# Kernel tuning notes

Hardware: AMD Instinct MI355X
Metric: run time of the kernel (lower is better)

Reference implementation:

```python
import jax, jax.numpy as jnp
import numpy as np

K, D_IN, D_OUT, R = 64, 256, 256, 64
TOK_PER_E = 4096
N_TOK = K * TOK_PER_E


def setup_inputs() -> dict:
    key = jax.random.key(0)
    k1, k2, k3, k4 = jax.random.split(key, 4)
    inp = jax.random.normal(k1, (N_TOK, D_IN), jnp.float32)
    # kaiming-uniform-ish scale for expert weights
    weight = jax.random.normal(k2, (K, D_OUT, D_IN), jnp.float32) * (1.0 / np.sqrt(D_IN))
    bias = jax.random.normal(k3, (K, D_OUT), jnp.float32) * 0.02
    # c_psuedo_inv built exactly as in __init__ from components [k, d, r]
    components = jax.random.normal(k4, (K, D_OUT, R), jnp.float32)
    gram = jnp.einsum('kdr,kds->krs', components, components)          # [k, r, r]
    c_inv = jnp.linalg.inv(gram)
    c_psuedo_inv = jnp.einsum('kdr,krs,kds->kds', components, c_inv, components)  # [k, d, d]
    fwd_expert_count = jnp.full((K,), TOK_PER_E, dtype=jnp.int32)
    return {
        'inp': inp,
        'fwd_expert_count': fwd_expert_count,
        'weight': weight,
        'bias': bias,
        'c_psuedo_inv': c_psuedo_inv,
        'max_tokens': TOK_PER_E,
    }


def reference(inp, fwd_expert_count, weight, bias, c_psuedo_inv, max_tokens):
    counts = fwd_expert_count                      # [k]
    k = counts.shape[0]
    n = inp.shape[0]
    offsets = jnp.concatenate([jnp.zeros((1,), counts.dtype), jnp.cumsum(counts)])  # [k+1]
    expert_ids = jnp.repeat(jnp.arange(k, dtype=counts.dtype), counts,
                            total_repeat_length=n)                                   # [n]
    token_pos = jnp.arange(n, dtype=counts.dtype) - offsets[expert_ids]              # [n]

    # Scatter ragged tokens into padded [k, max_tokens, in_feat], then do the
    # grouped linear as one batched GEMM (padded rows are zero; masked after bias).
    padded_in = jnp.zeros((k, max_tokens, inp.shape[1]), inp.dtype)
    padded_in = padded_in.at[expert_ids, token_pos].set(inp)
    x_pad = jnp.einsum('ktd,ked->kte', padded_in, weight) + bias[:, None, :]         # [k, t, e]
    valid = (jnp.arange(max_tokens)[None, :] < counts[:, None])[..., None]
    x_pad = jnp.where(valid, x_pad, jnp.zeros((), x_pad.dtype))

    padded = jnp.transpose(x_pad, (1, 0, 2))                                         # [t, k, e]
    return jnp.einsum('nkd,kds->nks', padded, c_psuedo_inv)                          # [t, k, e]
```

## Files before the change

kernel.cpp:

```cpp
#include <hip/hip_runtime.h>
#include <hip/hip_bf16.h>
#include <stdint.h>


typedef unsigned int   u32;
typedef unsigned short u16;

typedef short bf16x8 __attribute__((ext_vector_type(8)));
typedef float f32x4  __attribute__((ext_vector_type(4)));

__device__ __forceinline__ bf16x8 pack8(const float* v) {
  union { __hip_bfloat16 h[8]; bf16x8 v8; } r;
#pragma unroll
  for (int j = 0; j < 8; ++j) r.h[j] = __float2bfloat16(v[j]);
  return r.v8;
}
__device__ __forceinline__ u16 f2bf1(float f) {
  union { __hip_bfloat16 h; u16 u; } r;
  r.h = __float2bfloat16(f);
  return r.u;
}
__device__ __forceinline__ u32 pk2(float a, float b) {
  union { __hip_bfloat162 h; u32 u; } r;
  r.h.x = __float2bfloat16(a);
  r.h.y = __float2bfloat16(b);
  return r.u;
}
__device__ __forceinline__ void gload_lds16(const void* g, void* l) {
  __builtin_amdgcn_global_load_lds((__attribute__((address_space(1))) void*)g,
                                   (__attribute__((address_space(3))) void*)l,
                                   16, 0, 0);
}

__global__ __launch_bounds__(256, 2) void k_m(const float* __restrict__ P,
                                              const float* __restrict__ W,
                                              const float* __restrict__ bias,
                                              u16* __restrict__ Mt,
                                              float* __restrict__ b2) {
  const int k = blockIdx.y;
  const int tid = threadIdx.x;
  __shared__ __align__(16) unsigned char LDS[65536];
  const float* Pk = P + (size_t)k * 16384;

  if (blockIdx.x == 4) {
    const int sq = tid & 15, ec = tid >> 4;
    const float* bk = bias + k * 256;
    f32x4 acc = {};
#pragma unroll
    for (int i = 0; i < 16; ++i) {
      const int e = ec * 16 + i;
      const float4 pv = *reinterpret_cast<const float4*>(Pk + (size_t)e * 64 + sq * 4);
      const float bv = bk[e];
      acc[0] = fmaf(bv, pv.x, acc[0]);
      acc[1] = fmaf(bv, pv.y, acc[1]);
      acc[2] = fmaf(bv, pv.z, acc[2]);
      acc[3] = fmaf(bv, pv.w, acc[3]);
    }
    float* red = reinterpret_cast<float*>(LDS);
    *reinterpret_cast<f32x4*>(red + ec * 64 + sq * 4) = acc;
    __syncthreads();
    if (tid < 64) {
      float sum = 0.f;
#pragma unroll
      for (int c = 0; c < 16; ++c) sum += red[c * 64 + tid];
      b2[k * 64 + tid] = sum;
    }
    return;
  }

  const int d0 = blockIdx.x * 64;
  u32* WT = reinterpret_cast<u32*>(LDS);
  u32* PT = reinterpret_cast<u32*>(LDS + 32768);
  const float* Wk = W + (size_t)k * 65536;
  const int lane = tid & 63, w = tid >> 6, q = lane & 15, g = lane >> 4;

#pragma unroll
  for (int r = 0; r < 8; ++r) {
    const int ep = r * 16 + w * 4 + g;
    const float4 w0 = *reinterpret_cast<const float4*>(Wk + (size_t)(2 * ep) * 256 + d0 + 4 * q);
    const float4 w1 = *reinterpret_cast<const float4*>(Wk + (size_t)(2 * ep + 1) * 256 + d0 + 4 * q);
    const float4 p0 = *reinterpret_cast<const float4*>(Pk + (size_t)(2 * ep) * 64 + 4 * q);
    const float4 p1 = *reinterpret_cast<const float4*>(Pk + (size_t)(2 * ep + 1) * 64 + 4 * q);
    const int c = ep >> 2, cw = ep & 3;
    const float wa[4] = {w0.x, w0.y, w0.z, w0.w};
    const float wb[4] = {w1.x, w1.y, w1.z, w1.w};
    const float pa[4] = {p0.x, p0.y, p0.z, p0.w};
    const float pb[4] = {p1.x, p1.y, p1.z, p1.w};
#pragma unroll
    for (int j = 0; j < 4; ++j) {
      const int rw = 4 * q + j;
      const int sc = c ^ (rw & 7);
      WT[rw * 128 + sc * 4 + cw] = pk2(wa[j], wb[j]);
      PT[rw * 128 + sc * 4 + cw] = pk2(pa[j], pb[j]);
    }
  }
  __syncthreads();

  f32x4 acc[4] = {};
  const int dl = w * 16 + q;
#pragma unroll
  for (int kk = 0; kk < 8; ++kk) {
    const bf16x8 bfr = *reinterpret_cast<const bf16x8*>(
        reinterpret_cast<const char*>(WT) + dl * 512 + (((kk * 4 + g) ^ (dl & 7)) * 16));
#pragma unroll
    for (int m = 0; m < 4; ++m) {
      const int s = m * 16 + q;
      const bf16x8 afr = *reinterpret_cast<const bf16x8*>(
          reinterpret_cast<const char*>(PT) + s * 512 + (((kk * 4 + g) ^ (s & 7)) * 16));
      acc[m] = __builtin_amdgcn_mfma_f32_16x16x32_bf16(afr, bfr, acc[m], 0, 0, 0);
    }
  }
  u16* Mk = Mt + (size_t)k * 16384;
#pragma unroll
  for (int m = 0; m < 4; ++m)
#pragma unroll
    for (int j = 0; j < 4; ++j) {
      const int s = m * 16 + g * 4 + j;
      Mk[(size_t)s * 256 + d0 + w * 16 + q] = f2bf1(acc[m][j]);
    }
}

__global__ __launch_bounds__(256, 4) void k_main(const float* __restrict__ inp,
                                                 const u16* __restrict__ Mt,
                                                 const float* __restrict__ b2,
                                                 float* __restrict__ out) {
  const int tb = blockIdx.x, k = blockIdx.y;
  const int tid = threadIdx.x, lane = tid & 63, w = tid >> 6;
  __shared__ __align__(16) u16 Bl[16384];
  const u16* Mk = Mt + (size_t)k * 16384;
#pragma unroll
  for (int r = 0; r < 8; ++r) {
    const int q = r * 256 + tid;
    const int s = q >> 5, u = q & 31;
    gload_lds16(Mk + (size_t)s * 256 + ((u ^ (s & 7)) * 8),
                (char*)Bl + r * 4096 + w * 1024);
  }
  const float* Ak = inp + ((size_t)k * 4096 + tb * 256 + w * 64) * 256;
  f32x4 acc[4][4] = {};
  __syncthreads();

#pragma unroll
  for (int kk = 0; kk < 8; ++kk) {
    bf16x8 mt[4];
#pragma unroll
    for (int n = 0; n < 4; ++n) {
      const int s = n * 16 + (lane & 15);
      const int u = kk * 4 + (lane >> 4);
      mt[n] = *reinterpret_cast<const bf16x8*>(
          (const char*)Bl + s * 512 + ((u ^ (s & 7)) * 16));
    }
#pragma unroll
    for (int m = 0; m < 4; ++m) {
      const float* ap = Ak + (size_t)(m * 16 + (lane & 15)) * 256 +
                        kk * 32 + (lane >> 4) * 8;
      float va[8];
      *reinterpret_cast<float4*>(&va[0]) = *reinterpret_cast<const float4*>(ap);
      *reinterpret_cast<float4*>(&va[4]) = *reinterpret_cast<const float4*>(ap + 4);
      bf16x8 a = pack8(va);
#pragma unroll
      for (int n = 0; n < 4; ++n)
        acc[m][n] = __builtin_amdgcn_mfma_f32_16x16x32_bf16(mt[n], a, acc[m][n], 0, 0, 0);
    }
  }

  const float* b2k = b2 + k * 64;
  const int T0 = tb * 256 + w * 64;
  float4 bv[4];
#pragma unroll
  for (int n = 0; n < 4; ++n)
    bv[n] = *reinterpret_cast<const float4*>(b2k + n * 16 + (lane >> 4) * 4);
#pragma unroll
  for (int m = 0; m < 4; ++m) {
    const int t = T0 + m * 16 + (lane & 15);
    float* op = out + (size_t)t * 4096 + k * 64;
#pragma unroll
    for (int n = 0; n < 4; ++n) {
      float4 r;
      r.x = acc[m][n][0] + bv[n].x;
      r.y = acc[m][n][1] + bv[n].y;
      r.z = acc[m][n][2] + bv[n].z;
      r.w = acc[m][n][3] + bv[n].w;
      *reinterpret_cast<float4*>(op + n * 16 + (lane >> 4) * 4) = r;
    }
  }
}

extern "C" void kernel_launch(void* const* d_in, const int* in_sizes, int n_in,
                              void* d_out, int out_size, void* d_ws, size_t ws_size,
                              hipStream_t stream) {
  const float* inp  = (const float*)d_in[0];
  const float* W    = (const float*)d_in[2];
  const float* bias = (const float*)d_in[3];
  const float* P    = (const float*)d_in[4];

  u16*   Mm = (u16*)d_ws;
  float* b2 = (float*)((char*)d_ws + 2097152);
  float* o  = (float*)d_out;

  k_m   <<<dim3(5, 64),  256, 0, stream>>>(P, W, bias, Mm, b2);
  k_main<<<dim3(16, 64), 256, 0, stream>>>(inp, Mm, b2, o);
}
```

Measured before the change: 89.96 us.

## Stage input tiles through double-buffered LDS via async loads in main kernel

The main kernel now loads the fp32 input tile into LDS with global_load_lds, in 64-column chunks double-buffered across four stages, so the next chunk's fetch overlaps MFMA on the current one. Before, each lane issued direct global loads on the critical path. Each block now handles 64 tokens instead of 256, giving a 4x larger grid, a smaller accumulator, and 64KB of LDS per block with occupancy lowered to 2. The cost is a barrier per stage and the M matrix being reloaded into LDS four times as often overall.

```diff
diff --git a/kernel.cpp b/kernel.cpp
--- a/kernel.cpp
+++ b/kernel.cpp
@@ -120,68 +120,79 @@
     }
 }
 
-__global__ __launch_bounds__(256, 4) void k_main(const float* __restrict__ inp,
+__global__ __launch_bounds__(256, 2) void k_main(const float* __restrict__ inp,
                                                  const u16* __restrict__ Mt,
                                                  const float* __restrict__ b2,
                                                  float* __restrict__ out) {
   const int tb = blockIdx.x, k = blockIdx.y;
   const int tid = threadIdx.x, lane = tid & 63, w = tid >> 6;
-  __shared__ __align__(16) u16 Bl[16384];
+  const int q = lane & 15, g = lane >> 4;
+  __shared__ __align__(16) unsigned char LDS[65536];
+  u16* Bl = reinterpret_cast<u16*>(LDS);
+  unsigned char* const Ab[2] = {LDS + 32768, LDS + 49152};
+
   const u16* Mk = Mt + (size_t)k * 16384;
 #pragma unroll
   for (int r = 0; r < 8; ++r) {
-    const int q = r * 256 + tid;
-    const int s = q >> 5, u = q & 31;
+    const int qq = r * 256 + tid;
+    const int s = qq >> 5, u = qq & 31;
     gload_lds16(Mk + (size_t)s * 256 + ((u ^ (s & 7)) * 8),
                 (char*)Bl + r * 4096 + w * 1024);
   }
-  const float* Ak = inp + ((size_t)k * 4096 + tb * 256 + w * 64) * 256;
-  f32x4 acc[4][4] = {};
+
+  const float* Ak = inp + ((size_t)k * 4096 + (size_t)tb * 64) * 256;
+  auto stageA = [&](int c, unsigned char* A) {
+#pragma unroll
+    for (int r = 0; r < 4; ++r) {
+      const int tl = w * 16 + r * 4 + g;
+      gload_lds16(Ak + (size_t)tl * 256 + c * 64 + ((q ^ ((r * 4 + g) & 15)) * 4),
+                  A + (w * 16 + r * 4) * 256);
+    }
+  };
+
+  stageA(0, Ab[0]);
+  f32x4 acc[4] = {};
+  const int tl = w * 16 + q;
   __syncthreads();
 
 #pragma unroll
-  for (int kk = 0; kk < 8; ++kk) {
-    bf16x8 mt[4];
-#pragma unroll
-    for (int n = 0; n < 4; ++n) {
-      const int s = n * 16 + (lane & 15);
-      const int u = kk * 4 + (lane >> 4);
-      mt[n] = *reinterpret_cast<const bf16x8*>(
-          (const char*)Bl + s * 512 + ((u ^ (s & 7)) * 16));
-    }
-#pragma unroll
-    for (int m = 0; m < 4; ++m) {
-      const float* ap = Ak + (size_t)(m * 16 + (lane & 15)) * 256 +
-                        kk * 32 + (lane >> 4) * 8;
-      float va[8];
-      *reinterpret_cast<float4*>(&va[0]) = *reinterpret_cast<const float4*>(ap);
-      *reinterpret_cast<float4*>(&va[4]) = *reinterpret_cast<const float4*>(ap + 4);
-      bf16x8 a = pack8(va);
+  for (int c = 0; c < 4; ++c) {
+    if (c < 3) stageA(c + 1, Ab[(c + 1) & 1]);
+    const unsigned char* A = Ab[c & 1];
+#pragma unroll
+    for (int ks = 0; ks < 2; ++ks) {
+      const int kkg = c * 2 + ks;
+      bf16x8 mt[4];
+#pragma unroll
+      for (int n = 0; n < 4; ++n) {
+        const int s = n * 16 + q;
+        mt[n] = *reinterpret_cast<const bf16x8*>(
+            (const char*)Bl + s * 512 + (((kkg * 4 + g) ^ (s & 7)) * 16));
+      }
+      const int cg = ks * 8 + g * 2;
+      f32x4 v0 = *reinterpret_cast<const f32x4*>(A + tl * 256 + (((cg + 0) ^ q) * 16));
+      f32x4 v1 = *reinterpret_cast<const f32x4*>(A + tl * 256 + (((cg + 1) ^ q) * 16));
+      float va[8] = {v0[0], v0[1], v0[2], v0[3], v1[0], v1[1], v1[2], v1[3]};
+      const bf16x8 a = pack8(va);
 #pragma unroll
       for (int n = 0; n < 4; ++n)
-        acc[m][n] = __builtin_amdgcn_mfma_f32_16x16x32_bf16(mt[n], a, acc[m][n], 0, 0, 0);
-    }
+        acc[n] = __builtin_amdgcn_mfma_f32_16x16x32_bf16(mt[n], a, acc[n], 0, 0, 0);
+    }
+    __syncthreads();
   }
 
   const float* b2k = b2 + k * 64;
-  const int T0 = tb * 256 + w * 64;
-  float4 bv[4];
-#pragma unroll
-  for (int n = 0; n < 4; ++n)
-    bv[n] = *reinterpret_cast<const float4*>(b2k + n * 16 + (lane >> 4) * 4);
-#pragma unroll
-  for (int m = 0; m < 4; ++m) {
-    const int t = T0 + m * 16 + (lane & 15);
-    float* op = out + (size_t)t * 4096 + k * 64;
-#pragma unroll
-    for (int n = 0; n < 4; ++n) {
-      float4 r;
-      r.x = acc[m][n][0] + bv[n].x;
-      r.y = acc[m][n][1] + bv[n].y;
-      r.z = acc[m][n][2] + bv[n].z;
-      r.w = acc[m][n][3] + bv[n].w;
-      *reinterpret_cast<float4*>(op + n * 16 + (lane >> 4) * 4) = r;
-    }
+  const int t = tb * 64 + w * 16 + q;
+  float* op = out + (size_t)t * 4096 + k * 64;
+#pragma unroll
+  for (int n = 0; n < 4; ++n) {
+    const float4 bv = *reinterpret_cast<const float4*>(b2k + n * 16 + g * 4);
+    float4 r;
+    r.x = acc[n][0] + bv.x;
+    r.y = acc[n][1] + bv.y;
+    r.z = acc[n][2] + bv.z;
+    r.w = acc[n][3] + bv.w;
+    *reinterpret_cast<float4*>(op + n * 16 + g * 4) = r;
   }
 }
 
@@ -198,5 +209,5 @@
   float* o  = (float*)d_out;
 
   k_m   <<<dim3(5, 64),  256, 0, stream>>>(P, W, bias, Mm, b2);
-  k_main<<<dim3(16, 64), 256, 0, stream>>>(inp, Mm, b2, o);
-}
+  k_main<<<dim3(64, 64), 256, 0, stream>>>(inp, Mm, b2, o);
+}
```

Result: no change. 89.90 us (-0.1%).
